# Kernel optimization log

Measured on AMD Instinct MI355X. Metric: run time of the kernel, lower is better.

The kernel has to match this reference:

```python
import jax, jax.numpy as jnp
import numpy as np

B, LQ, LA, H = 32, 1024, 1024, 512
NEG = -1e7


def setup_inputs() -> dict:
    key = jax.random.key(0)
    kq, ka, ku = jax.random.split(key, 3)
    q = jax.random.normal(kq, (B, LQ, H), dtype=jnp.float32)
    a = jax.random.normal(ka, (B, LA, H), dtype=jnp.float32)
    U = 0.02 * jax.random.normal(ku, (H, H), dtype=jnp.float32)  # init.normal(std=0.02)
    q_mask = jnp.ones((B, LQ, 1), dtype=jnp.float32)
    a_mask = jnp.ones((B, LA, 1), dtype=jnp.float32)
    return {"q": q, "a": a, "U": U, "q_mask": q_mask, "a_mask": a_mask}


def reference(q, a, U, q_mask, a_mask):
    # mask[b,i,j] = q_mask[b,i] * a_mask[b,j]  (nonzero => valid)
    mask = jnp.matmul(q_mask, jnp.swapaxes(a_mask, 1, 2)) > 0  # [B,LQ,LA] bool
    # bilinear score X = q @ U @ a^T
    qU = jnp.einsum('bqh,hk->bqk', q, U)
    X = jnp.einsum('bqk,bak->bqa', qU, a)  # [B,LQ,LA]
    X = jnp.where(mask, X, NEG)
    I = jax.nn.sigmoid(X)
    att_a2q = jnp.max(jax.nn.softmax(I, axis=-1), axis=-1)  # [B,LQ]
    att_q2a = jnp.max(jax.nn.softmax(I, axis=-2), axis=-2)  # [B,LA]
    q_attn = jnp.einsum('blh,bl->bh', q, att_a2q)  # [B,H]
    a_attn = jnp.einsum('blh,bl->bh', a, att_q2a)  # [B,H]
    return q_attn, a_attn
```

## Files before the change

### kernel.cpp

```cpp
#include <hip/hip_runtime.h>

typedef __attribute__((ext_vector_type(8))) short bf16x8;
typedef __attribute__((ext_vector_type(4))) float f32x4;
typedef unsigned short u16;
typedef unsigned int u32;

#define NLOG2E -1.44269504088896f
#define LOG2E   1.44269504088896f
#define SLICE 32768

__device__ __forceinline__ float bf2f(u16 x) {
  union { u32 u; float f; } v; v.u = ((u32)x) << 16; return v.f;
}
__device__ __forceinline__ u16 f2b(float f) {
  union { float f; u32 u; } v; v.f = f;
  return (u16)((v.u + 0x7FFFu + ((v.u >> 16) & 1u)) >> 16);
}
__device__ __forceinline__ u32 pk2(float lo, float hi) {
  return (u32)f2b(lo) | ((u32)f2b(hi) << 16);
}
__device__ __forceinline__ bool inputs_are_bf16(const void* qmask) {
  return *(const u32*)qmask == 0x3F803F80u;
}

__global__ __launch_bounds__(256) void prep_all(
    const void* __restrict__ q, const void* __restrict__ a,
    const void* __restrict__ U, const void* __restrict__ qmask,
    u16* __restrict__ qb, u16* __restrict__ ab, u16* __restrict__ Ut,
    float* __restrict__ out)
{
  const bool bf = inputs_are_bf16(qmask);
  const int t = threadIdx.x;
  if (blockIdx.x < 64) {
    const int bb = blockIdx.x;
    out[bb * 512 + t] = 0.f;
    out[bb * 512 + 256 + t] = 0.f;
    __shared__ u16 tile[64][65];
    const int bx = bb & 7, by = bb >> 3;
    #pragma unroll
    for (int i = 0; i < 16; i++) {
      int r = i * 4 + (t >> 6);
      int c = t & 63;
      size_t gi = (size_t)(by * 64 + r) * 512 + bx * 64 + c;
      tile[c][r] = bf ? ((const u16*)U)[gi] : f2b(((const float*)U)[gi]);
    }
    __syncthreads();
    #pragma unroll
    for (int i = 0; i < 16; i++) {
      int r = i * 4 + (t >> 6);
      int c = t & 63;
      Ut[(size_t)(bx * 64 + r) * 512 + by * 64 + c] = tile[r][c];
    }
  } else {
    if (bf) return;
    const int bi = blockIdx.x - 64;
    const bool isq = bi < 4096;
    const int idx = (isq ? bi : bi - 4096) * 256 + t;
    const float4* s = (const float4*)(isq ? q : a) + (size_t)idx * 4;
    float4 v0 = s[0], v1 = s[1], v2 = s[2], v3 = s[3];
    uint4* d = (uint4*)(isq ? qb : ab) + (size_t)idx * 2;
    uint4 w0, w1;
    w0.x = pk2(v0.x, v0.y); w0.y = pk2(v0.z, v0.w);
    w0.z = pk2(v1.x, v1.y); w0.w = pk2(v1.z, v1.w);
    w1.x = pk2(v2.x, v2.y); w1.y = pk2(v2.z, v2.w);
    w1.z = pk2(v3.x, v3.y); w1.w = pk2(v3.z, v3.w);
    d[0] = w0;
    d[1] = w1;
  }
}

template<int EPI>
__global__ __launch_bounds__(256, 2) void gemm_bt(
    const u16* __restrict__ A, const u16* __restrict__ B,
    u16* __restrict__ C, float scaleC,
    size_t strideA, size_t strideB,
    const void* __restrict__ q_mask, const void* __restrict__ a_mask,
    float* __restrict__ statsP,
    const u16* __restrict__ A_alias, const u16* __restrict__ B_alias)
{
  __shared__ __align__(16) char smem[66560];
  u16* Ct  = (u16*)smem;
  float* redS = (float*)smem;
  float* redM = (float*)(smem + 16896);
  float* colS = (float*)(smem + 33792);
  float* colM = (float*)(smem + 34816);
  float* qp = (float*)(smem + 65536);
  float* ap = (float*)(smem + 66048);

  const int bx = blockIdx.x, by = blockIdx.y, bz = blockIdx.z;
  const int tid  = threadIdx.x;
  const int lane = tid & 63;
  const int wave = tid >> 6;
  const int wr = wave >> 1, wc = wave & 1;
  const int l15 = lane & 15, lq = lane >> 4;

  const bool bfin = inputs_are_bf16(q_mask);
  const u16* Asel = (bfin && A_alias) ? A_alias : A;
  const u16* Bsel = (bfin && B_alias) ? B_alias : B;

  const int srl  = lane >> 2;
  const int sc   = (lane & 3) ^ ((lane >> 3) & 3);
  const size_t sgo = (size_t)srl * 512 + sc * 8;
  const int foff = ((lq ^ ((l15 >> 1) & 3)) * 8);

  const u16* Ab = Asel + strideA * bz + (size_t)by * 128 * 512;
  const u16* Bb = Bsel + strideB * bz + (size_t)bx * 128 * 512;

  if (EPI) {
    if (tid < 128) {
      int gi = bz * 1024 + by * 128 + tid;
      float v = bfin ? bf2f(((const u16*)q_mask)[gi]) : ((const float*)q_mask)[gi];
      qp[tid] = (v > 0.f) ? 0.f : 1e30f;
    } else {
      int gj = bz * 1024 + bx * 128 + (tid - 128);
      float v = bfin ? bf2f(((const u16*)a_mask)[gj]) : ((const float*)a_mask)[gj];
      ap[tid - 128] = (v > 0.f) ? 0.f : 1e30f;
    }
    __syncthreads();
  }

  f32x4 acc[4][4];
  if (EPI) {
    #pragma unroll
    for (int mt = 0; mt < 4; mt++)
      #pragma unroll
      for (int nt = 0; nt < 4; nt++) {
        float cp = ap[wc * 64 + nt * 16 + l15];
        #pragma unroll
        for (int r = 0; r < 4; r++)
          acc[mt][nt][r] = qp[wr * 64 + mt * 16 + lq * 4 + r] + cp;
      }
  } else {
    #pragma unroll
    for (int i = 0; i < 4; i++)
      #pragma unroll
      for (int j = 0; j < 4; j++) {
        f32x4 z = {0.f, 0.f, 0.f, 0.f};
        acc[i][j] = z;
      }
  }

  auto stage32 = [&](int buf, int k0) {
    char* base = smem + buf * 16384;
    #pragma unroll
    for (int i = 0; i < 2; i++) {
      const size_t go = (size_t)(wave * 32 + i * 16) * 512 + k0 + sgo;
      __builtin_amdgcn_global_load_lds(
          (const __attribute__((address_space(1))) void*)(Ab + go),
          (__attribute__((address_space(3))) void*)(base + wave * 2048 + i * 1024), 16, 0, 0);
      __builtin_amdgcn_global_load_lds(
          (const __attribute__((address_space(1))) void*)(Bb + go),
          (__attribute__((address_space(3))) void*)(base + 8192 + wave * 2048 + i * 1024), 16, 0, 0);
    }
  };

  stage32(0, 0);
  stage32(1, 32);
  stage32(2, 64);
  #pragma unroll
  for (int t = 0; t < 16; t++) {
    if (t + 3 < 16) stage32((t + 3) & 3, (t + 3) * 32);
    if (t < 13)      asm volatile("s_waitcnt vmcnt(12)\n\ts_barrier" ::: "memory");
    else if (t == 13) asm volatile("s_waitcnt vmcnt(8)\n\ts_barrier" ::: "memory");
    else if (t == 14) asm volatile("s_waitcnt vmcnt(4)\n\ts_barrier" ::: "memory");
    else              asm volatile("s_waitcnt vmcnt(0)\n\ts_barrier" ::: "memory");

    const u16* As = (const u16*)(smem + (t & 3) * 16384);
    const u16* Bs = (const u16*)(smem + (t & 3) * 16384 + 8192);
    bf16x8 af[4], bfr[4];
    #pragma unroll
    for (int tt = 0; tt < 4; tt++) {
      const int ar = wr * 64 + tt * 16 + l15;
      const int br = wc * 64 + tt * 16 + l15;
      af[tt]  = *(const bf16x8*)&As[ar * 32 + foff];
      bfr[tt] = *(const bf16x8*)&Bs[br * 32 + foff];
    }
    #pragma unroll
    for (int mt = 0; mt < 4; mt++)
      #pragma unroll
      for (int nt = 0; nt < 4; nt++)
        acc[mt][nt] = __builtin_amdgcn_mfma_f32_16x16x32_bf16(af[mt], bfr[nt], acc[mt][nt], 0, 0, 0);
    asm volatile("s_waitcnt lgkmcnt(0)\n\ts_barrier" ::: "memory");
  }

  if (!EPI) {
    #pragma unroll
    for (int mt = 0; mt < 4; mt++)
      #pragma unroll
      for (int nt = 0; nt < 4; nt++)
        #pragma unroll
        for (int r = 0; r < 4; r++) {
          int row = wr * 64 + mt * 16 + lq * 4 + r;
          int col = wc * 64 + nt * 16 + l15;
          Ct[row * 144 + col] = f2b(scaleC * acc[mt][nt][r]);
        }
    __syncthreads();
    u16* Cb = C + (size_t)by * 128 * 512 + bx * 128;
    #pragma unroll
    for (int i = 0; i < 8; i++) {
      int c = tid + i * 256;
      int row = c >> 4, cc = c & 15;
      *(bf16x8*)&Cb[(size_t)row * 512 + cc * 8] = *(const bf16x8*)&Ct[row * 144 + cc * 8];
    }
  } else {
    const int gi0 = bz * 1024 + by * 128;
    const int gj0 = bz * 1024 + bx * 128;
    float* rowsumP = statsP + 0      + bx * SLICE;
    float* colsumP = statsP + 262144 + by * SLICE;
    float* rowminP = statsP + 524288 + bx * SLICE;
    float* colminP = statsP + 786432 + by * SLICE;

    float csum[4] = {0.f, 0.f, 0.f, 0.f};
    float cmin[4] = {3e38f, 3e38f, 3e38f, 3e38f};
    #pragma unroll
    for (int mt = 0; mt < 4; mt++) {
      #pragma unroll
      for (int r = 0; r < 4; r++) {
        const int row = wr * 64 + mt * 16 + lq * 4 + r;
        float rsm = 0.f, rmn = 3e38f;
        #pragma unroll
        for (int nt = 0; nt < 4; nt++) {
          float y = acc[mt][nt][r];
          float u = __builtin_amdgcn_exp2f(y);
          float s = __builtin_amdgcn_rcpf(1.f + u);
          float e = __builtin_amdgcn_exp2f(LOG2E * s);
          rsm += e;
          csum[nt] += e;
          rmn = fminf(rmn, y);
          cmin[nt] = fminf(cmin[nt], y);
        }
        redS[row * 33 + l15 + 16 * wc] = rsm;
        redM[row * 33 + l15 + 16 * wc] = rmn;
      }
    }
    #pragma unroll
    for (int nt = 0; nt < 4; nt++) {
      float cs = csum[nt], cm = cmin[nt];
      cs += __shfl_xor(cs, 16); cm = fminf(cm, __shfl_xor(cm, 16));
      cs += __shfl_xor(cs, 32); cm = fminf(cm, __shfl_xor(cm, 32));
      if (lane < 16) {
        int j = wc * 64 + nt * 16 + l15;
        colS[j * 2 + wr] = cs;
        colM[j * 2 + wr] = cm;
      }
    }
    __syncthreads();
    if (tid < 128) {
      float s = 0.f;
      #pragma unroll
      for (int j = 0; j < 32; j++) s += redS[tid * 33 + j];
      rowsumP[gi0 + tid] = s;
      colsumP[gj0 + tid] = colS[tid * 2] + colS[tid * 2 + 1];
    } else {
      const int r = tid - 128;
      float m = 3e38f;
      #pragma unroll
      for (int j = 0; j < 32; j++) m = fminf(m, redM[r * 33 + j]);
      rowminP[gi0 + r] = m;
      colminP[gj0 + r] = fminf(colM[r * 2], colM[r * 2 + 1]);
    }
  }
}

__global__ __launch_bounds__(256) void partial_kernel(
    const u16* __restrict__ qb, const u16* __restrict__ ab,
    const void* __restrict__ q0, const void* __restrict__ a0,
    const void* __restrict__ qmask,
    const float* __restrict__ statsP, float* __restrict__ out)
{
  __shared__ float att[128];
  const int tid = threadIdx.x;
  const int seg = blockIdx.x;
  const int b = blockIdx.y >> 1, half = blockIdx.y & 1;
  if (tid < 128) {
    const int g = b * 1024 + seg * 128 + tid;
    const float* sumP = statsP + half * 262144;
    const float* minP = statsP + 524288 + half * 262144;
    float s = 0.f, m = 3e38f;
    #pragma unroll
    for (int s8 = 0; s8 < 8; s8++) {
      s += sumP[s8 * SLICE + g];
      m = fminf(m, minP[s8 * SLICE + g]);
    }
    float Imax = __builtin_amdgcn_rcpf(1.f + __builtin_amdgcn_exp2f(m));
    att[tid] = __expf(Imax) * __builtin_amdgcn_rcpf(s);
  }
  __syncthreads();
  const bool bf = inputs_are_bf16(qmask);
  const u16* base = bf ? (const u16*)(half ? a0 : q0) : (half ? ab : qb);
  const u32* src = (const u32*)(base + (size_t)b * 524288
                                + (size_t)seg * 128 * 512);
  float a0v = 0.f, a1v = 0.f;
  #pragma unroll 8
  for (int i = 0; i < 128; i++) {
    u32 w = src[i * 256 + tid];
    float wt = att[i];
    a0v = fmaf(__uint_as_float(w << 16), wt, a0v);
    a1v = fmaf(__uint_as_float(w & 0xFFFF0000u), wt, a1v);
  }
  float* ob = out + half * 16384 + b * 512 + tid * 2;
  atomicAdd(&ob[0], a0v);
  atomicAdd(&ob[1], a1v);
}

extern "C" void kernel_launch(void* const* d_in, const int* in_sizes, int n_in,
                              void* d_out, int out_size, void* d_ws, size_t ws_size,
                              hipStream_t stream) {
  const void* q  = d_in[0];
  const void* a  = d_in[1];
  const void* U  = d_in[2];
  const void* qm = d_in[3];
  const void* am = d_in[4];
  float* out = (float*)d_out;

  char* ws = (char*)d_ws;
  u16* qb    = (u16*)ws;
  u16* ab    = (u16*)(ws + 33554432);
  u16* qU    = (u16*)(ws + 67108864);
  u16* Ut    = (u16*)(ws + 100663296);
  float* statsP = (float*)(ws + 100663296);

  const int prep_blocks = (in_sizes[0] == 33554432) ? 64 : 8256;
  prep_all<<<dim3(prep_blocks), dim3(256), 0, stream>>>(q, a, U, qm, qb, ab, Ut, out);
  gemm_bt<0><<<dim3(4, 256, 1), dim3(256), 0, stream>>>(
      qb, Ut, qU, NLOG2E, (size_t)0, (size_t)0, qm, am, statsP,
      (const u16*)q, (const u16*)nullptr);
  gemm_bt<1><<<dim3(8, 8, 32), dim3(256), 0, stream>>>(
      qU, ab, (u16*)nullptr, 1.f, (size_t)524288, (size_t)524288, qm, am, statsP,
      (const u16*)nullptr, (const u16*)a);
  partial_kernel<<<dim3(8, 64), dim3(256), 0, stream>>>(qb, ab, q, a, qm, statsP, out);
}
```

Baseline: 245.6 us.

## Shrink GEMM LDS ring to three stages, remap epilogue blocks, vectorize partial reduction

The GEMM's LDS ring buffer goes from four 16KB stages to three, cutting shared memory from about 65KB to about 49KB and raising launch bounds to 3 blocks per CU. The prefetch depth drops from 3 to 2 tiles in exchange for the extra occupancy. For the EPI variant, block indices are remapped so neighbouring blocks share A/B tiles, aiming at better L2 reuse. The partial_kernel now loads 16 bytes per thread across 4 row groups and reduces them in shared memory instead of doing 4-byte strided loads.

```diff
diff --git a/kernel.cpp b/kernel.cpp
--- a/kernel.cpp
+++ b/kernel.cpp
@@ -70,7 +70,7 @@
 }
 
 template<int EPI>
-__global__ __launch_bounds__(256, 2) void gemm_bt(
+__global__ __launch_bounds__(256, 3) void gemm_bt(
     const u16* __restrict__ A, const u16* __restrict__ B,
     u16* __restrict__ C, float scaleC,
     size_t strideA, size_t strideB,
@@ -78,16 +78,22 @@
     float* __restrict__ statsP,
     const u16* __restrict__ A_alias, const u16* __restrict__ B_alias)
 {
-  __shared__ __align__(16) char smem[66560];
+  __shared__ __align__(16) char smem[50176];
   u16* Ct  = (u16*)smem;
   float* redS = (float*)smem;
   float* redM = (float*)(smem + 16896);
   float* colS = (float*)(smem + 33792);
   float* colM = (float*)(smem + 34816);
-  float* qp = (float*)(smem + 65536);
-  float* ap = (float*)(smem + 66048);
-
-  const int bx = blockIdx.x, by = blockIdx.y, bz = blockIdx.z;
+  float* qp = (float*)(smem + 49152);
+  float* ap = (float*)(smem + 49664);
+
+  int bx = blockIdx.x, by = blockIdx.y;
+  const int bz = blockIdx.z;
+  if (EPI) {
+    const int k = blockIdx.x, s = blockIdx.y;
+    bx = (k & 3) * 2 + (s & 1);
+    by = (k >> 2) * 4 + (s >> 1);
+  }
   const int tid  = threadIdx.x;
   const int lane = tid & 63;
   const int wave = tid >> 6;
@@ -156,17 +162,15 @@
 
   stage32(0, 0);
   stage32(1, 32);
-  stage32(2, 64);
   #pragma unroll
   for (int t = 0; t < 16; t++) {
-    if (t + 3 < 16) stage32((t + 3) & 3, (t + 3) * 32);
-    if (t < 13)      asm volatile("s_waitcnt vmcnt(12)\n\ts_barrier" ::: "memory");
-    else if (t == 13) asm volatile("s_waitcnt vmcnt(8)\n\ts_barrier" ::: "memory");
+    if (t + 2 < 16) stage32((t + 2) % 3, (t + 2) * 32);
+    if (t <= 13)      asm volatile("s_waitcnt vmcnt(8)\n\ts_barrier" ::: "memory");
     else if (t == 14) asm volatile("s_waitcnt vmcnt(4)\n\ts_barrier" ::: "memory");
     else              asm volatile("s_waitcnt vmcnt(0)\n\ts_barrier" ::: "memory");
 
-    const u16* As = (const u16*)(smem + (t & 3) * 16384);
-    const u16* Bs = (const u16*)(smem + (t & 3) * 16384 + 8192);
+    const u16* As = (const u16*)(smem + (t % 3) * 16384);
+    const u16* Bs = (const u16*)(smem + (t % 3) * 16384 + 8192);
     bf16x8 af[4], bfr[4];
     #pragma unroll
     for (int tt = 0; tt < 4; tt++) {
@@ -269,6 +273,7 @@
     const float* __restrict__ statsP, float* __restrict__ out)
 {
   __shared__ float att[128];
+  __shared__ float red[4][512];
   const int tid = threadIdx.x;
   const int seg = blockIdx.x;
   const int b = blockIdx.y >> 1, half = blockIdx.y & 1;
@@ -288,19 +293,35 @@
   __syncthreads();
   const bool bf = inputs_are_bf16(qmask);
   const u16* base = bf ? (const u16*)(half ? a0 : q0) : (half ? ab : qb);
-  const u32* src = (const u32*)(base + (size_t)b * 524288
-                                + (size_t)seg * 128 * 512);
-  float a0v = 0.f, a1v = 0.f;
+  const uint4* src = (const uint4*)(base + (size_t)b * 524288
+                                    + (size_t)seg * 128 * 512);
+  const int rw = tid >> 6;
+  const int lane = tid & 63;
+  float a0v = 0.f, a1v = 0.f, a2v = 0.f, a3v = 0.f;
+  float a4v = 0.f, a5v = 0.f, a6v = 0.f, a7v = 0.f;
   #pragma unroll 8
-  for (int i = 0; i < 128; i++) {
-    u32 w = src[i * 256 + tid];
-    float wt = att[i];
-    a0v = fmaf(__uint_as_float(w << 16), wt, a0v);
-    a1v = fmaf(__uint_as_float(w & 0xFFFF0000u), wt, a1v);
-  }
-  float* ob = out + half * 16384 + b * 512 + tid * 2;
-  atomicAdd(&ob[0], a0v);
-  atomicAdd(&ob[1], a1v);
+  for (int i = 0; i < 32; i++) {
+    const int row = i * 4 + rw;
+    uint4 w = src[(size_t)row * 64 + lane];
+    float wt = att[row];
+    a0v = fmaf(__uint_as_float(w.x << 16), wt, a0v);
+    a1v = fmaf(__uint_as_float(w.x & 0xFFFF0000u), wt, a1v);
+    a2v = fmaf(__uint_as_float(w.y << 16), wt, a2v);
+    a3v = fmaf(__uint_as_float(w.y & 0xFFFF0000u), wt, a3v);
+    a4v = fmaf(__uint_as_float(w.z << 16), wt, a4v);
+    a5v = fmaf(__uint_as_float(w.z & 0xFFFF0000u), wt, a5v);
+    a6v = fmaf(__uint_as_float(w.w << 16), wt, a6v);
+    a7v = fmaf(__uint_as_float(w.w & 0xFFFF0000u), wt, a7v);
+  }
+  *(float4*)&red[rw][lane * 8]     = make_float4(a0v, a1v, a2v, a3v);
+  *(float4*)&red[rw][lane * 8 + 4] = make_float4(a4v, a5v, a6v, a7v);
+  __syncthreads();
+  const int h = tid * 2;
+  float s0 = red[0][h]     + red[1][h]     + red[2][h]     + red[3][h];
+  float s1 = red[0][h + 1] + red[1][h + 1] + red[2][h + 1] + red[3][h + 1];
+  float* ob = out + half * 16384 + b * 512 + h;
+  atomicAdd(&ob[0], s0);
+  atomicAdd(&ob[1], s1);
 }
 
 extern "C" void kernel_launch(void* const* d_in, const int* in_sizes, int n_in,
```

Measured after the change: 237.8 us. -3.2%, faster.
